# Kernel optimization log

Hardware: AMD Instinct MI355X
Metric: run time of the kernel (lower is better)

## Reference

```python
import jax, jax.numpy as jnp
import numpy as np

INPUT_DIM = 512
OUTPUT_DIM = 512
GRID_SIZE = 16
INPUT_MIN = -1.0
INPUT_RANGE = 2.0


def setup_inputs() -> dict:
    key = jax.random.key(0)
    k_x, k_mix = jax.random.split(key)
    x = jax.random.normal(k_x, (65536, INPUT_DIM), dtype=jnp.float32)
    # per-dim spline tables: bases init zeros, slopes init 0.1 (as in torch)
    bases = jnp.zeros((INPUT_DIM, GRID_SIZE), dtype=jnp.float32)
    slopes = jnp.full((INPUT_DIM, GRID_SIZE), 0.1, dtype=jnp.float32)
    mix = jax.random.normal(k_mix, (OUTPUT_DIM, INPUT_DIM), dtype=jnp.float32) * 0.01
    bias = jnp.zeros((OUTPUT_DIM,), dtype=jnp.float32)
    return {"x": x, "bases": bases, "slopes": slopes, "mix": mix, "bias": bias}


def reference(x, bases, slopes, mix, bias):
    # x: [B, D]; bases/slopes: [D, G]; mix: [O, D]; bias: [O]
    B, D = x.shape
    G = bases.shape[1]
    x_norm = jnp.clip((x - INPUT_MIN) / INPUT_RANGE, 0.0, 1.0 - 1e-6)
    idx = jnp.clip((x_norm * G).astype(jnp.int32), 0, G - 1)        # [B, D]
    x_local = x_norm * G - idx.astype(x.dtype)                       # fractional position in cell
    # gather per-dim table entries: flatten [D, G] and index with d*G + idx
    flat_idx = jnp.arange(D, dtype=jnp.int32)[None, :] * G + idx    # [B, D]
    base = bases.reshape(-1)[flat_idx]                               # [B, D]
    slope = slopes.reshape(-1)[flat_idx]                             # [B, D]
    spline_out = base + slope * x_local                              # [B, D]
    y = jnp.einsum('bd,od->bo', spline_out, mix) + bias              # [B, O]
    return y
```

## Files before the change

### kernel.cpp

```cpp
#include <hip/hip_runtime.h>


#define DIMK 512
#define DIMN 512
#define GRID_G 16

typedef unsigned short u16;
typedef unsigned int u32;
typedef __attribute__((ext_vector_type(8))) __bf16 bf16x8;
typedef __attribute__((ext_vector_type(4))) float f32x4;

__device__ __forceinline__ u32 bf16rne(float f) {
    u32 u = __float_as_uint(f);
    return (u + 0x7fffu + ((u >> 16) & 1u)) >> 16;
}

__global__ void prep_kernel(const float* __restrict__ mix,
                            const float* __restrict__ bases,
                            const float* __restrict__ slopes,
                            u16* __restrict__ mixb,
                            float2* __restrict__ tab) {
    int t = blockIdx.x * 256 + threadIdx.x;
    float4 v = reinterpret_cast<const float4*>(mix)[t];
    ushort4 o;
    o.x = (u16)bf16rne(v.x);
    o.y = (u16)bf16rne(v.y);
    o.z = (u16)bf16rne(v.z);
    o.w = (u16)bf16rne(v.w);
    reinterpret_cast<ushort4*>(mixb)[t] = o;
    if (t < DIMK * GRID_G) {
        tab[t] = make_float2(bases[t], slopes[t]);
    }
}

__global__ __launch_bounds__(512, 2) void kan_kernel(
    const float* __restrict__ x, const float2* __restrict__ tab,
    const u16* __restrict__ mixb, const float* __restrict__ bias,
    float* __restrict__ y) {
    __shared__ __align__(16) u16 sA[128 * 32];
    __shared__ __align__(16) u16 sB[512 * 32];

    const int tid = threadIdx.x;
    const int lane = tid & 63;
    const int wid = tid >> 6;
    const int quad = lane >> 4;
    const int l15 = lane & 15;
    const int wave_m = wid >> 2;
    const int wave_n = wid & 3;
    const int m0 = blockIdx.x * 128;

    const int ar = tid >> 2;
    const int akg = tid & 3;
    const int awchunk = (ar << 2) | (akg ^ ((ar >> 1) & 3));
    const float4* xrow =
        reinterpret_cast<const float4*>(x + (size_t)(m0 + ar) * DIMK) + akg * 2;

    f32x4 acc[4][8];
#pragma unroll
    for (int i = 0; i < 4; i++)
#pragma unroll
        for (int j = 0; j < 8; j++) acc[i][j] = (f32x4){0.f, 0.f, 0.f, 0.f};

    float4 xa = xrow[0];
    float4 xb = xrow[1];

    for (int kt = 0; kt < 16; ++kt) {
        float xs[8] = {xa.x, xa.y, xa.z, xa.w, xb.x, xb.y, xb.z, xb.w};
        const int dbase = kt * 32 + akg * 8;
        float2 bs[8];
        float tv[8];
        int idxv[8];
#pragma unroll
        for (int j = 0; j < 8; j++) {
            float xn = fminf(fmaxf((xs[j] + 1.0f) * 0.5f, 0.0f), 0.999999f);
            float tt = xn * 16.0f;
            int idx = (int)tt;
            if (idx > 15) idx = 15;
            tv[j] = tt;
            idxv[j] = idx;
            bs[j] = tab[((dbase + j) << 4) + idx];
        }
        u32 h[8];
#pragma unroll
        for (int j = 0; j < 8; j++) {
            float sp = bs[j].x + bs[j].y * (tv[j] - (float)idxv[j]);
            h[j] = bf16rne(sp);
        }
        int4 pk = make_int4((int)(h[0] | (h[1] << 16)), (int)(h[2] | (h[3] << 16)),
                            (int)(h[4] | (h[5] << 16)), (int)(h[6] | (h[7] << 16)));
        *reinterpret_cast<int4*>(&sA[awchunk * 8]) = pk;

#pragma unroll
        for (int i = 0; i < 4; i++) {
            int grp = wid * 4 + i;
            int n = grp * 16 + (lane >> 2);
            int c = (lane & 3) ^ ((n >> 1) & 3);
            const u16* gsrc = mixb + (size_t)n * DIMK + kt * 32 + c * 8;
            __builtin_amdgcn_global_load_lds(
                (const __attribute__((address_space(1))) void*)gsrc,
                (__attribute__((address_space(3))) void*)(&sB[grp * 512]),
                16, 0, 0);
        }
        __syncthreads();

        if (kt < 15) {
            xa = xrow[(kt + 1) * 8];
            xb = xrow[(kt + 1) * 8 + 1];
        }

        bf16x8 afrag[4];
#pragma unroll
        for (int fm = 0; fm < 4; fm++) {
            int m_l = wave_m * 64 + fm * 16 + l15;
            int ci = (m_l << 2) | (quad ^ ((m_l >> 1) & 3));
            afrag[fm] = *reinterpret_cast<const bf16x8*>(&sA[ci * 8]);
        }
#pragma unroll
        for (int fn = 0; fn < 8; fn++) {
            int n_l = wave_n * 128 + fn * 16 + l15;
            int ci = (n_l << 2) | (quad ^ ((n_l >> 1) & 3));
            bf16x8 bfrag = *reinterpret_cast<const bf16x8*>(&sB[ci * 8]);
#pragma unroll
            for (int fm = 0; fm < 4; fm++)
                acc[fm][fn] = __builtin_amdgcn_mfma_f32_16x16x32_bf16(
                    afrag[fm], bfrag, acc[fm][fn], 0, 0, 0);
        }
        __syncthreads();
    }

#pragma unroll
    for (int fn = 0; fn < 8; fn++) {
        int o = wave_n * 128 + fn * 16 + l15;
        float bv = bias[o];
#pragma unroll
        for (int fm = 0; fm < 4; fm++) {
            int row = m0 + wave_m * 64 + fm * 16 + quad * 4;
            float* yp = y + (size_t)row * DIMN + o;
#pragma unroll
            for (int j = 0; j < 4; j++)
                yp[(size_t)j * DIMN] = acc[fm][fn][j] + bv;
        }
    }
}

extern "C" void kernel_launch(void* const* d_in, const int* in_sizes, int n_in,
                              void* d_out, int out_size, void* d_ws, size_t ws_size,
                              hipStream_t stream) {
    const float* x = (const float*)d_in[0];
    const float* bases = (const float*)d_in[1];
    const float* slopes = (const float*)d_in[2];
    const float* mix = (const float*)d_in[3];
    const float* bias = (const float*)d_in[4];
    float* y = (float*)d_out;

    u16* mixb = (u16*)d_ws;
    float2* tab = (float2*)((char*)d_ws + 512 * 1024);

    hipLaunchKernelGGL(prep_kernel, dim3(256), dim3(256), 0, stream,
                       mix, bases, slopes, mixb, tab);
    hipLaunchKernelGGL(kan_kernel, dim3(512), dim3(512), 0, stream,
                       x, tab, mixb, bias, y);
}
```

Measured before the change: 277.7 us.

## Stage spline tables in LDS as packed bf16 pairs per block

The kernel no longer gathers base/slope pairs from global memory through a prepared float2 table. Each block now loads the full per-dimension table into shared memory at startup, packing base and slope as two bf16 values in one word, and pads each row to 17 entries to avoid bank conflicts. Inner-loop gathers then become LDS reads, and the prep kernel no longer builds the table. The cost is an extra 34KB of LDS per block, which may limit occupancy, plus a per-block prologue of 16 loads per thread. Storing base and slope in bf16 before the spline evaluation adds rounding error compared with the fp32 table.

```diff
diff --git a/kernel.cpp b/kernel.cpp
--- a/kernel.cpp
+++ b/kernel.cpp
@@ -16,10 +16,7 @@
 }
 
 __global__ void prep_kernel(const float* __restrict__ mix,
-                            const float* __restrict__ bases,
-                            const float* __restrict__ slopes,
-                            u16* __restrict__ mixb,
-                            float2* __restrict__ tab) {
+                            u16* __restrict__ mixb) {
     int t = blockIdx.x * 256 + threadIdx.x;
     float4 v = reinterpret_cast<const float4*>(mix)[t];
     ushort4 o;
@@ -28,15 +25,13 @@
     o.z = (u16)bf16rne(v.z);
     o.w = (u16)bf16rne(v.w);
     reinterpret_cast<ushort4*>(mixb)[t] = o;
-    if (t < DIMK * GRID_G) {
-        tab[t] = make_float2(bases[t], slopes[t]);
-    }
 }
 
 __global__ __launch_bounds__(512, 2) void kan_kernel(
-    const float* __restrict__ x, const float2* __restrict__ tab,
-    const u16* __restrict__ mixb, const float* __restrict__ bias,
-    float* __restrict__ y) {
+    const float* __restrict__ x, const float* __restrict__ bases,
+    const float* __restrict__ slopes, const u16* __restrict__ mixb,
+    const float* __restrict__ bias, float* __restrict__ y) {
+    __shared__ u32 s_tab[DIMK * 17];
     __shared__ __align__(16) u16 sA[128 * 32];
     __shared__ __align__(16) u16 sB[512 * 32];
 
@@ -48,6 +43,13 @@
     const int wave_m = wid >> 2;
     const int wave_n = wid & 3;
     const int m0 = blockIdx.x * 128;
+
+#pragma unroll
+    for (int k = 0; k < 16; k++) {
+        int i = tid + k * 512;
+        u32 p = bf16rne(bases[i]) | (bf16rne(slopes[i]) << 16);
+        s_tab[(i >> 4) * 17 + (i & 15)] = p;
+    }
 
     const int ar = tid >> 2;
     const int akg = tid & 3;
@@ -64,26 +66,21 @@
     float4 xa = xrow[0];
     float4 xb = xrow[1];
 
+    __syncthreads();
+
     for (int kt = 0; kt < 16; ++kt) {
         float xs[8] = {xa.x, xa.y, xa.z, xa.w, xb.x, xb.y, xb.z, xb.w};
         const int dbase = kt * 32 + akg * 8;
-        float2 bs[8];
-        float tv[8];
-        int idxv[8];
+        u32 h[8];
 #pragma unroll
         for (int j = 0; j < 8; j++) {
             float xn = fminf(fmaxf((xs[j] + 1.0f) * 0.5f, 0.0f), 0.999999f);
             float tt = xn * 16.0f;
             int idx = (int)tt;
-            if (idx > 15) idx = 15;
-            tv[j] = tt;
-            idxv[j] = idx;
-            bs[j] = tab[((dbase + j) << 4) + idx];
-        }
-        u32 h[8];
-#pragma unroll
-        for (int j = 0; j < 8; j++) {
-            float sp = bs[j].x + bs[j].y * (tv[j] - (float)idxv[j]);
+            u32 p = s_tab[(dbase + j) * 17 + idx];
+            float base = __uint_as_float(p << 16);
+            float slope = __uint_as_float(p & 0xffff0000u);
+            float sp = fmaf(slope, tt - (float)idx, base);
             h[j] = bf16rne(sp);
         }
         int4 pk = make_int4((int)(h[0] | (h[1] << 16)), (int)(h[2] | (h[3] << 16)),
@@ -154,10 +151,8 @@
     float* y = (float*)d_out;
 
     u16* mixb = (u16*)d_ws;
-    float2* tab = (float2*)((char*)d_ws + 512 * 1024);
 
-    hipLaunchKernelGGL(prep_kernel, dim3(256), dim3(256), 0, stream,
-                       mix, bases, slopes, mixb, tab);
+    hipLaunchKernelGGL(prep_kernel, dim3(256), dim3(256), 0, stream, mix, mixb);
     hipLaunchKernelGGL(kan_kernel, dim3(512), dim3(512), 0, stream,
-                       x, tab, mixb, bias, y);
+                       x, bases, slopes, mixb, bias, y);
 }
```

New measurement: 263.5 us. 1.05x faster.
